# Kernel optimization log

Hardware: AMD Instinct MI355X
Metric: run time of the kernel (lower is better)

## Reference

```python
import jax, jax.numpy as jnp
import numpy as np

ND, NPR, DD, DP, LAT, AT, B = 2048, 2048, 128, 128, 128, 32, 16384


def setup_inputs():
    key = jax.random.key(0)
    ks = jax.random.split(key, 20)
    s = 0.05
    d = {}
    d["e_p_adj"] = (jax.random.uniform(ks[0], (ND, NPR)) < 0.05).astype(jnp.float32)
    d["e_e_adj"] = (jax.random.uniform(ks[1], (ND, ND)) < 0.05).astype(jnp.float32)
    d["p_p_adj"] = (jax.random.uniform(ks[2], (NPR, NPR)) < 0.05).astype(jnp.float32)
    d["input_disease"] = jax.random.randint(ks[3], (B,), 0, ND)
    d["input_drug"] = jax.random.randint(ks[4], (B,), 0, NPR)
    d["labels"] = jax.random.randint(ks[5], (B,), 0, 2)
    # learned parameters
    d["disease_emb"] = jax.random.normal(ks[6], (ND, DD)) * s
    d["drug_emb"] = jax.random.normal(ks[7], (NPR, DP)) * s
    d["Wdg"] = jax.random.normal(ks[8], (DP, LAT)) * s   # disease_gcn_w
    d["bdg_lin"] = jnp.zeros((LAT,))                      # Linear bias
    d["bdg"] = jnp.zeros((LAT,))                          # extra disease_gcn_b
    d["Wpg"] = jax.random.normal(ks[9], (DD, LAT)) * s   # drug_gcn_w
    d["bpg_lin"] = jnp.zeros((LAT,))
    d["bpg"] = jnp.zeros((LAT,))
    d["Wa1_d"] = jax.random.normal(ks[10], (DP + DD, AT)) * s  # concat [key(drug), query(disease)]
    d["ba1_d"] = jnp.zeros((AT,))
    d["Wa2_d"] = jax.random.normal(ks[11], (AT, 1)) * s
    d["ba2_d"] = jnp.zeros((1,))
    d["Wa1_p"] = jax.random.normal(ks[12], (DD + DP, AT)) * s  # concat [key(disease), query(drug)]
    d["ba1_p"] = jnp.zeros((AT,))
    d["Wa2_p"] = jax.random.normal(ks[13], (AT, 1)) * s
    d["ba2_p"] = jnp.zeros((1,))
    d["Wd2"] = jax.random.normal(ks[14], (DD, LAT)) * s  # disease_w2
    d["bd2"] = jnp.zeros((LAT,))
    d["Wp3"] = jax.random.normal(ks[15], (DP, LAT)) * s  # drug_w3
    d["bp3"] = jnp.zeros((LAT,))
    d["mlp_W1"] = jax.random.normal(ks[16], (LAT, DD)) * s
    d["mlp_b1"] = jnp.zeros((DD,))
    d["mlp_W2"] = jax.random.normal(ks[17], (DD, DD)) * s
    d["mlp_b2"] = jnp.zeros((DD,))
    d["Wpred"] = jax.random.normal(ks[18], (DD, 1)) * s
    d["bpred"] = jnp.zeros((1,))
    return d


def _attention_gcn(adj, other, selfe, W1, b1, W2, b2):
    # torch: concat([key=other, query=self]) -> Linear(W1) ; split W1 instead of
    # materializing the [Ns, No, Dk+Dq] concat tensor (same math, less HBM traffic)
    do = other.shape[1]
    ko = other @ W1[:do]              # [No, A]
    qs = selfe @ W1[do:]              # [Ns, A]
    h = jax.nn.relu(qs[:, None, :] + ko[None, :, :] + b1)   # [Ns, No, A]
    alpha = jax.nn.relu(jnp.squeeze(h @ W2, -1) + b2[0])    # [Ns, No]
    alpha = alpha * adj
    return jax.nn.softmax(alpha, axis=1) @ other            # [Ns, Do]


def _forward(e_p_adj, e_e_adj, p_p_adj, input_disease, input_drug, labels,
             disease_emb, drug_emb, Wdg, bdg_lin, bdg, Wpg, bpg_lin, bpg,
             Wa1_d, ba1_d, Wa2_d, ba2_d, Wa1_p, ba1_p, Wa2_p, ba2_p,
             Wd2, bd2, Wp3, bp3, mlp_W1, mlp_b1, mlp_W2, mlp_b2, Wpred, bpred):
    h_e_gcn = _attention_gcn(e_p_adj, drug_emb, disease_emb, Wa1_d, ba1_d, Wa2_d, ba2_d)
    h_e_gcn = h_e_gcn @ Wdg + bdg_lin + bdg
    h_p_gcn = _attention_gcn(e_p_adj.T, disease_emb, drug_emb, Wa1_p, ba1_p, Wa2_p, ba2_p)
    h_p_gcn = h_p_gcn @ Wpg + bpg_lin + bpg
    # disease knn branch
    deg_d = jnp.sum(e_e_adj, axis=1, keepdims=True) + 1e-8
    h_e_e = ((e_e_adj @ disease_emb) / deg_d) @ Wd2 + bd2
    h_e = jax.nn.selu(h_e_gcn + h_e_e)
    # drug knn branch
    deg_p = jnp.sum(p_p_adj, axis=1, keepdims=True) + 1e-8
    h_p_p = ((p_p_adj @ drug_emb) / deg_p) @ Wp3 + bp3
    h_p = jax.nn.selu(h_p_gcn + h_p_p)
    # pair prediction MLP
    x = h_e[input_disease] * h_p[input_drug]                # [B, LAT]
    x = jax.nn.selu(x @ mlp_W1 + mlp_b1)
    x = jax.nn.selu(x @ mlp_W2 + mlp_b2)
    z = jnp.squeeze(x @ Wpred, -1) + bpred[0]               # [B]
    y = labels.astype(jnp.float32)
    # BCEWithLogitsLoss (stable), mean reduction
    loss = jnp.mean(jnp.maximum(z, 0.0) - z * y + jnp.log1p(jnp.exp(-jnp.abs(z))))
    return (loss, jax.nn.sigmoid(z))


def reference(e_p_adj, e_e_adj, p_p_adj, input_disease, input_drug, labels,
              disease_emb, drug_emb, Wdg, bdg_lin, bdg, Wpg, bpg_lin, bpg,
              Wa1_d, ba1_d, Wa2_d, ba2_d, Wa1_p, ba1_p, Wa2_p, ba2_p,
              Wd2, bd2, Wp3, bp3, mlp_W1, mlp_b1, mlp_W2, mlp_b2, Wpred, bpred):
    return _forward(e_p_adj, e_e_adj, p_p_adj, input_disease, input_drug, labels,
                    disease_emb, drug_emb, Wdg, bdg_lin, bdg, Wpg, bpg_lin, bpg,
                    Wa1_d, ba1_d, Wa2_d, ba2_d, Wa1_p, ba1_p, Wa2_p, ba2_p,
                    Wd2, bd2, Wp3, bp3, mlp_W1, mlp_b1, mlp_W2, mlp_b2, Wpred, bpred)
```

## Files before the change

### kernel.cpp

```cpp
#include <hip/hip_runtime.h>

#define ND   2048
#define BB   16384

typedef unsigned short u16;
typedef unsigned int u32;
typedef __attribute__((ext_vector_type(8))) short short8;
typedef __attribute__((ext_vector_type(4))) float f32x4;

__device__ inline float bf2f(u16 u) {
    union { u32 i; float f; } v; v.i = ((u32)u) << 16; return v.f;
}
__device__ inline u16 f2bf(float f) {
    union { float f; u32 i; } v; v.f = f;
    u32 i = v.i + 0x7fffu + ((v.i >> 16) & 1u);
    return (u16)(i >> 16);
}
__device__ inline float seluf(float x) {
    const float sc = 1.0507009873554805f, al = 1.6732632423543772f;
    return x > 0.f ? sc * x : sc * al * expm1f(x);
}

__global__ void detectk(const void* __restrict__ demb, u32* __restrict__ flag,
                        u32* __restrict__ cntT, float* __restrict__ lossacc,
                        u32* __restrict__ losscnt) {
    const u16* p = (const u16*)demb;
    int tid = threadIdx.x;
    #pragma unroll
    for (int i = 0; i < 8; i++) cntT[i * 256 + tid] = 0u;
    if (tid == 0) { lossacc[0] = 0.f; losscnt[0] = 0u; }
    int sane = 0;
    #pragma unroll
    for (int i = 0; i < 2; i++) {
        u16 u = p[4 * tid + 2 * i];
        int e = (u >> 7) & 0xFF;
        if (u == 0 || (e >= 0x66 && e <= 0x8C)) sane++;
    }
    __shared__ int red[256];
    red[tid] = sane; __syncthreads();
    for (int o = 128; o > 0; o >>= 1) {
        if (tid < o) red[tid] += red[tid + o];
        __syncthreads();
    }
    if (tid == 0) flag[0] = (red[0] < 300) ? 1u : 0u;
}

#define NSEG 26
struct CvtArgs { const void* src[NSEG]; int off[NSEG]; int n[NSEG]; };
struct CS {
    const void* adj[3];
    u16* ridx[3]; u32* rcnt[3];
};

__global__ __launch_bounds__(256) void cvtcsr(CvtArgs a, u16* __restrict__ base,
                                              CS c, const u32* __restrict__ flag) {
    int bx = blockIdx.x;
    int t = threadIdx.x;
    bool f32 = flag[0] != 0;
    if (bx < 1536) {
        int m = bx >> 9;
        int r0 = (bx & 511) * 4;
        int lane = t & 63;
        __shared__ u32 lcnt[4];
        if (t < 4) lcnt[t] = 0;
        __syncthreads();
        float v[4][8];
        int c0 = t * 8;
        if (f32) {
            #pragma unroll
            for (int rr = 0; rr < 4; rr++) {
                const float4* p = (const float4*)((const float*)c.adj[m] +
                                                  (size_t)(r0 + rr) * 2048 + c0);
                float4 x = p[0], y = p[1];
                v[rr][0] = x.x; v[rr][1] = x.y; v[rr][2] = x.z; v[rr][3] = x.w;
                v[rr][4] = y.x; v[rr][5] = y.y; v[rr][6] = y.z; v[rr][7] = y.w;
            }
        } else {
            #pragma unroll
            for (int rr = 0; rr < 4; rr++) {
                const uint4* p = (const uint4*)((const u16*)c.adj[m] +
                                                (size_t)(r0 + rr) * 2048 + c0);
                uint4 x = p[0];
                u32 u[4] = {x.x, x.y, x.z, x.w};
                #pragma unroll
                for (int i = 0; i < 4; i++) {
                    v[rr][2 * i + 0] = (u[i] & 0xffffu) ? 1.f : 0.f;
                    v[rr][2 * i + 1] = (u[i] >> 16)     ? 1.f : 0.f;
                }
            }
        }
        #pragma unroll
        for (int rr = 0; rr < 4; rr++) {
            int cnt = 0;
            #pragma unroll
            for (int i = 0; i < 8; i++) cnt += (v[rr][i] != 0.f) ? 1 : 0;
            int pfx = cnt;
            #pragma unroll
            for (int o = 1; o < 64; o <<= 1) {
                int s = __shfl_up(pfx, o, 64);
                if (lane >= o) pfx += s;
            }
            int wtot = __shfl(pfx, 63, 64);
            u32 wb = 0;
            if (lane == 0) wb = atomicAdd(&lcnt[rr], (u32)wtot);
            wb = __shfl((int)wb, 0, 64);
            int o = (int)wb + pfx - cnt;
            u16* ridx = c.ridx[m] + (size_t)(r0 + rr) * 2048;
            #pragma unroll
            for (int i = 0; i < 8; i++) {
                if (v[rr][i] != 0.f) ridx[o++] = (u16)(c0 + i);
            }
        }
        __syncthreads();
        if (t < 4) c.rcnt[m][r0 + t] = lcnt[t];
    } else {
        int idx = bx - 1536;
        int seg = idx >> 6, xb = idx & 63;
        int n = a.n[seg];
        const void* s = a.src[seg];
        u16* d = base + a.off[seg];
        for (int i = xb * 256 + t; i < n; i += 16384)
            d[i] = f32 ? f2bf(((const float*)s)[i]) : ((const u16*)s)[i];
    }
}

struct PR {
    const u16* demb; const u16* pemb;
    const u16* Wa1d; const u16* ba1d;
    const u16* Wa1p; const u16* ba1p;
    float* ko_d; float* qs_d; float* ko_p; float* qs_p;
    const u16* idx0; const u32* cnt0; u16* cidx; u32* ccnt;
    const u16* ts[6]; u16* W1T; u16* W2T; u16* WcTe; u16* WcTp;
    const u16* ba[3]; const u16* bb[3]; u16* b_e; u16* b_p;
    float* csd; float* csp;
    const u16* avgidx[2]; const u32* avgcnt[2]; const u16* avgemb[2]; u16* avgout[2];
};

__global__ __launch_bounds__(256) void prep2(PR p) {
    int bx = blockIdx.x;
    int tid = threadIdx.x;
    __shared__ float sx[2][128];
    __shared__ float sred[2][128];
    __shared__ u16 stile[32][33];
    __shared__ float st0[256], st1[256];

    if (bx < 4096) {
        int sub = tid >> 7, t = tid & 127;
        int unit = bx * 2 + sub;
        int row = unit & 2047, m = unit >> 11;
        const u16* src; const u16* W; const u16* bias; float* out;
        switch (m) {
            case 0:  src = p.pemb; W = p.Wa1d;            bias = nullptr; out = p.ko_d; break;
            case 1:  src = p.demb; W = p.Wa1d + 128 * 32; bias = p.ba1d;  out = p.qs_d; break;
            case 2:  src = p.demb; W = p.Wa1p;            bias = nullptr; out = p.ko_p; break;
            default: src = p.pemb; W = p.Wa1p + 128 * 32; bias = p.ba1p;  out = p.qs_p; break;
        }
        sx[sub][t] = bf2f(src[(size_t)row * 128 + t]);
        __syncthreads();
        int a = t & 31, part = t >> 5;
        float s = 0.f;
        #pragma unroll
        for (int k = 0; k < 32; k++)
            s += sx[sub][part * 32 + k] * bf2f(W[(part * 32 + k) * 32 + a]);
        sred[sub][t] = s;
        __syncthreads();
        if (part == 0) {
            float tt = sred[sub][a] + sred[sub][a + 32] + sred[sub][a + 64] + sred[sub][a + 96];
            if (bias) tt += bf2f(bias[a]);
            out[(size_t)row * 32 + a] = tt;
        }
    } else if (bx < 6144) {
        int r = bx - 4096;
        int n = (int)p.cnt0[r];
        const u16* row = p.idx0 + (size_t)r * 2048;
        for (int i = tid; i < n; i += 256) {
            int cc = (int)row[i];
            u32 q = atomicAdd(&p.ccnt[cc], 1u);
            p.cidx[(size_t)cc * 2048 + q] = (u16)r;
        }
    } else if (bx < 6240) {
        int id = bx - 6144;
        int z = id >> 4, rem = id & 15;
        int c0 = (rem & 3) * 32, r0 = (rem >> 2) * 32;
        const u16* in = p.ts[z];
        u16* out; int ldo, ooff;
        switch (z) {
            case 0:  out = p.W1T;  ldo = 128; ooff = 0;   break;
            case 1:  out = p.W2T;  ldo = 128; ooff = 0;   break;
            case 2:  out = p.WcTe; ldo = 256; ooff = 0;   break;
            case 3:  out = p.WcTe; ldo = 256; ooff = 128; break;
            case 4:  out = p.WcTp; ldo = 256; ooff = 0;   break;
            default: out = p.WcTp; ldo = 256; ooff = 128; break;
        }
        int tx = tid & 31, ty = tid >> 5;
        int x = c0 + tx;
        for (int i = ty; i < 32; i += 8)
            stile[i][tx] = in[(size_t)(r0 + i) * 128 + x];
        __syncthreads();
        int rr = r0 + tx;
        for (int i = ty; i < 32; i += 8)
            out[(size_t)(c0 + i) * ldo + ooff + rr] = stile[tx][i];
    } else if (bx < 7264) {
        int id = bx - 6240;
        int task = id >> 9, blk = id & 511;
        int wv = tid >> 6, lane = tid & 63;
        int grp = lane >> 4, dim = lane & 15;
        int r = blk * 4 + wv;
        const u16* idx = p.avgidx[task] + (size_t)r * 2048;
        int nnz = (int)p.avgcnt[task][r];
        const u16* emb = p.avgemb[task];
        float acc[8];
        #pragma unroll
        for (int t = 0; t < 8; t++) acc[t] = 0.f;
        for (int base = 0; base < nnz; base += 64) {
            int i = base + lane;
            int j = (i < nnz) ? (int)idx[i] : 0;
            int cend = min(64, nnz - base);
            #pragma unroll 4
            for (int k4 = 0; k4 < cend; k4 += 4) {
                int kk = k4 + grp;
                int jk = __shfl(j, kk, 64);
                float wk = (base + kk < nnz) ? 1.f : 0.f;
                const uint4* pp = (const uint4*)((const char*)emb + jk * 256 + dim * 16);
                uint4 vv = *pp;
                u32 u[4] = {vv.x, vv.y, vv.z, vv.w};
                #pragma unroll
                for (int cc = 0; cc < 4; cc++) {
                    acc[2 * cc + 0] = fmaf(wk, bf2f((u16)(u[cc] & 0xffffu)), acc[2 * cc + 0]);
                    acc[2 * cc + 1] = fmaf(wk, bf2f((u16)(u[cc] >> 16)), acc[2 * cc + 1]);
                }
            }
        }
        #pragma unroll
        for (int t = 0; t < 8; t++) {
            acc[t] += __shfl_xor(acc[t], 32, 64);
            acc[t] += __shfl_xor(acc[t], 16, 64);
        }
        if (grp == 0) {
            float sc = 1.f / ((float)nnz + 1e-8f);
            float v[8];
            #pragma unroll
            for (int t = 0; t < 8; t++) v[t] = acc[t] * sc;
            uint4 pk;
            pk.x = (u32)f2bf(v[0]) | ((u32)f2bf(v[1]) << 16);
            pk.y = (u32)f2bf(v[2]) | ((u32)f2bf(v[3]) << 16);
            pk.z = (u32)f2bf(v[4]) | ((u32)f2bf(v[5]) << 16);
            pk.w = (u32)f2bf(v[6]) | ((u32)f2bf(v[7]) << 16);
            *(uint4*)(p.avgout[task] + (size_t)r * 256 + dim * 8) = pk;
        }
    } else {
        int id = bx - 7264;
        int m = id >> 1, half = id & 1;
        const u16* e = m ? p.pemb : p.demb;
        int c2 = tid & 31, rg = tid >> 5;
        int dbase = half * 64;
        float s0 = 0.f, s1 = 0.f;
        for (int it = 0; it < 256; it++) {
            int row = it * 8 + rg;
            u32 v = *(const u32*)(e + (size_t)row * 128 + dbase + c2 * 2);
            s0 += bf2f((u16)(v & 0xffffu));
            s1 += bf2f((u16)(v >> 16));
        }
        st0[tid] = s0; st1[tid] = s1;
        __syncthreads();
        if (tid < 32) {
            float a0 = 0.f, a1 = 0.f;
            #pragma unroll
            for (int g = 0; g < 8; g++) { a0 += st0[g * 32 + tid]; a1 += st1[g * 32 + tid]; }
            float* cs = m ? p.csp : p.csd;
            cs[dbase + tid * 2 + 0] = a0;
            cs[dbase + tid * 2 + 1] = a1;
        }
        if (tid < 64) {
            int d = dbase + tid;
            if (m == 0)
                p.b_e[d] = f2bf(bf2f(p.ba[0][d]) + bf2f(p.ba[1][d]) + bf2f(p.ba[2][d]));
            else
                p.b_p[d] = f2bf(bf2f(p.bb[0][d]) + bf2f(p.bb[1][d]) + bf2f(p.bb[2][d]));
        }
    }
}

struct SP {
    const u16* idx[2]; const u32* cnt[2];
    const float* ko[2]; const float* qs[2];
    const u16* w2[2]; const u16* b2[2];
    const u16* emb[2]; const float* csum[2];
    u16* out[2];
};

__global__ __launch_bounds__(256) void spagg(SP a) {
    int task = blockIdx.y;
    int tid = threadIdx.x;
    int wv = tid >> 6, lane = tid & 63;
    int grp = lane >> 4, dim = lane & 15;
    int r = blockIdx.x * 4 + wv;
    const u16* idx = a.idx[task] + (size_t)r * 2048;
    int nnz = (int)a.cnt[task][r];
    const u16* emb = a.emb[task];
    const float* ko = a.ko[task];

    float qsr[32], w2h[32];
    {
        const float4* qp = (const float4*)(a.qs[task] + (size_t)r * 32);
        #pragma unroll
        for (int i = 0; i < 8; i++) {
            float4 v = qp[i];
            qsr[4 * i + 0] = v.x; qsr[4 * i + 1] = v.y;
            qsr[4 * i + 2] = v.z; qsr[4 * i + 3] = v.w;
        }
        #pragma unroll
        for (int i = 0; i < 32; i++) w2h[i] = bf2f(a.w2[task][i]);
    }
    float b2v = bf2f(a.b2[task][0]);

    float acc[8];
    #pragma unroll
    for (int t = 0; t < 8; t++) acc[t] = 0.f;
    float wsuml = 0.f;

    for (int base = 0; base < nnz; base += 64) {
        int i = base + lane;
        float w = 0.f;
        int j = 0;
        if (i < nnz) {
            j = (int)idx[i];
            const float4* kp = (const float4*)(ko + (size_t)j * 32);
            float s = 0.f;
            #pragma unroll
            for (int q = 0; q < 8; q++) {
                float4 kv = kp[q];
                s += fmaxf(qsr[4 * q + 0] + kv.x, 0.f) * w2h[4 * q + 0];
                s += fmaxf(qsr[4 * q + 1] + kv.y, 0.f) * w2h[4 * q + 1];
                s += fmaxf(qsr[4 * q + 2] + kv.z, 0.f) * w2h[4 * q + 2];
                s += fmaxf(qsr[4 * q + 3] + kv.w, 0.f) * w2h[4 * q + 3];
            }
            w = __expf(fmaxf(s + b2v, 0.f)) - 1.f;
            wsuml += w;
        }
        int cend = min(64, nnz - base);
        #pragma unroll 4
        for (int k4 = 0; k4 < cend; k4 += 4) {
            int kk = k4 + grp;
            float wk = __shfl(w, kk, 64);
            int jk = __shfl(j, kk, 64);
            const uint4* pp = (const uint4*)((const char*)emb + jk * 256 + dim * 16);
            uint4 vv = *pp;
            u32 u[4] = {vv.x, vv.y, vv.z, vv.w};
            #pragma unroll
            for (int cc = 0; cc < 4; cc++) {
                acc[2 * cc + 0] = fmaf(wk, bf2f((u16)(u[cc] & 0xffffu)), acc[2 * cc + 0]);
                acc[2 * cc + 1] = fmaf(wk, bf2f((u16)(u[cc] >> 16)), acc[2 * cc + 1]);
            }
        }
    }

    #pragma unroll
    for (int t = 0; t < 8; t++) {
        acc[t] += __shfl_xor(acc[t], 32, 64);
        acc[t] += __shfl_xor(acc[t], 16, 64);
    }
    #pragma unroll
    for (int o = 32; o > 0; o >>= 1) wsuml += __shfl_xor(wsuml, o, 64);

    if (grp == 0) {
        float sc = 1.f / (2048.f + wsuml);
        const float* cs = a.csum[task] + dim * 8;
        float v[8];
        #pragma unroll
        for (int t = 0; t < 8; t++) v[t] = (cs[t] + acc[t]) * sc;
        uint4 pk;
        pk.x = (u32)f2bf(v[0]) | ((u32)f2bf(v[1]) << 16);
        pk.y = (u32)f2bf(v[2]) | ((u32)f2bf(v[3]) << 16);
        pk.z = (u32)f2bf(v[4]) | ((u32)f2bf(v[5]) << 16);
        pk.w = (u32)f2bf(v[6]) | ((u32)f2bf(v[7]) << 16);
        *(uint4*)(a.out[task] + (size_t)r * 256 + dim * 8) = pk;
    }
}

struct GD4 {
    const void* A[4]; const u16* BT[4]; u16* C[4];
    const u16* bias[4]; const float* rs[4];
    int lda[4], ldb[4], ldc[4], coff[4], kiters[4], act[4], araw[4], rsmode[4];
};

#define PADK 136

__global__ __launch_bounds__(256, 2) void gemmL(GD4 g, const u32* __restrict__ flag) {
    __shared__ __align__(16) u16 As[16][PADK];
    __shared__ __align__(16) u16 Bs[128][PADK];
    int z = blockIdx.y;
    const void* A = g.A[z];
    const u16* BT = g.BT[z];
    int lda = g.lda[z], ldb = g.ldb[z];
    int kiters = g.kiters[z];
    int tid = threadIdx.x;
    int lane = tid & 63, wv = tid >> 6;
    int mrow = lane & 15, quad = lane >> 4;
    int m0 = blockIdx.x * 16;
    int c0 = wv * 32;
    int sr = tid >> 4, sk = (tid & 15) * 8;
    f32x4 acc0 = {0.f, 0.f, 0.f, 0.f}, acc1 = {0.f, 0.f, 0.f, 0.f};

    short8 ra, rb[8];
    auto ldstage = [&](int kb) {
        ra = *(const short8*)((const u16*)A + (size_t)(m0 + sr) * lda + kb + sk);
        const u16* bbase = BT + (size_t)sr * ldb + kb + sk;
        #pragma unroll
        for (int i = 0; i < 8; i++)
            rb[i] = *(const short8*)(bbase + (size_t)i * 16 * ldb);
    };
    auto ststage = [&]() {
        *(short8*)(&As[sr][sk]) = ra;
        #pragma unroll
        for (int i = 0; i < 8; i++)
            *(short8*)(&Bs[i * 16 + sr][sk]) = rb[i];
    };
    auto compute = [&]() {
        #pragma unroll
        for (int ks = 0; ks < 4; ks++) {
            short8 af = *(const short8*)(&As[mrow][ks * 32 + quad * 8]);
            short8 b0 = *(const short8*)(&Bs[c0 + mrow][ks * 32 + quad * 8]);
            short8 b1 = *(const short8*)(&Bs[c0 + 16 + mrow][ks * 32 + quad * 8]);
            acc0 = __builtin_amdgcn_mfma_f32_16x16x32_bf16(af, b0, acc0, 0, 0, 0);
            acc1 = __builtin_amdgcn_mfma_f32_16x16x32_bf16(af, b1, acc1, 0, 0, 0);
        }
    };

    ldstage(0);
    #pragma unroll 1
    for (int it = 0; it < kiters - 1; ++it) {
        ststage();
        __syncthreads();
        ldstage((it + 1) * 128);
        compute();
        __syncthreads();
    }
    ststage();
    __syncthreads();
    compute();

    const float* rs = g.rs[z];
    int rsmode = g.rsmode[z];
    const u16* bi = g.bias[z];
    u16* C = g.C[z];
    int ldc = g.ldc[z], coff = g.coff[z], act = g.act[z];
    int n0 = c0 + mrow, n1 = n0 + 16;
    float bv0 = bi ? bf2f(bi[n0]) : 0.f;
    float bv1 = bi ? bf2f(bi[n1]) : 0.f;
    #pragma unroll
    for (int r = 0; r < 4; r++) {
        int row = m0 + quad * 4 + r;
        float v0 = acc0[r], v1 = acc1[r];
        if (rsmode == 1) { float sc = rs[row]; v0 *= sc; v1 *= sc; }
        else if (rsmode == 2) {
            float t = 0.f;
            #pragma unroll
            for (int p = 0; p < 8; p++) t += rs[row + p * 2048];
            float sc = 1.f / t;
            v0 *= sc; v1 *= sc;
        }
        v0 += bv0; v1 += bv1;
        if (act) { v0 = seluf(v0); v1 = seluf(v1); }
        C[(size_t)row * ldc + coff + n0] = f2bf(v0);
        C[(size_t)row * ldc + coff + n1] = f2bf(v1);
    }
}

#define PADX 136
__global__ __launch_bounds__(256, 2) void mlpfused(
    const u16* __restrict__ he, const u16* __restrict__ hp,
    const int* __restrict__ di, const int* __restrict__ dr,
    const u16* __restrict__ W1T, const u16* __restrict__ b1,
    const u16* __restrict__ W2T, const u16* __restrict__ b2,
    const u16* __restrict__ wpred, const u16* __restrict__ bpred,
    const int* __restrict__ labels,
    float* __restrict__ out, float* __restrict__ lossacc,
    u32* __restrict__ losscnt) {
    __shared__ __align__(16) u16 Xs[64][PADX];
    __shared__ __align__(16) u16 Ws[128][PADX];
    __shared__ float wred[4];
    int tid = threadIdx.x;
    int lane = tid & 63, wv = tid >> 6;
    int mrow = lane & 15, quad = lane >> 4;
    int p0 = blockIdx.x * 64;

    {
        int row = tid >> 2, sub = tid & 3;
        int b = p0 + row;
        int ia = di[b], ic = dr[b];
        const uint4* pe = (const uint4*)(he + (size_t)ia * 128 + sub * 32);
        const uint4* pp = (const uint4*)(hp + (size_t)ic * 128 + sub * 32);
        #pragma unroll
        for (int q = 0; q < 4; q++) {
            uint4 ue = pe[q], up = pp[q];
            u32 eu[4] = {ue.x, ue.y, ue.z, ue.w};
            u32 pu[4] = {up.x, up.y, up.z, up.w};
            #pragma unroll
            for (int c = 0; c < 4; c++) {
                float lo = bf2f((u16)(eu[c] & 0xffffu)) * bf2f((u16)(pu[c] & 0xffffu));
                float hi = bf2f((u16)(eu[c] >> 16)) * bf2f((u16)(pu[c] >> 16));
                *(u32*)(&Xs[row][sub * 32 + q * 8 + c * 2]) =
                    (u32)f2bf(lo) | ((u32)f2bf(hi) << 16);
            }
        }
    }
    {
        int n = tid >> 1, half = tid & 1;
        const short8* src = (const short8*)(W1T + (size_t)n * 128 + half * 64);
        short8* dst = (short8*)(&Ws[n][half * 64]);
        #pragma unroll
        for (int i = 0; i < 8; i++) dst[i] = src[i];
    }
    __syncthreads();

    f32x4 acc[8];
    #pragma unroll
    for (int nt = 0; nt < 8; nt++) acc[nt] = {0.f, 0.f, 0.f, 0.f};
    #pragma unroll
    for (int ks = 0; ks < 4; ks++) {
        short8 af = *(const short8*)(&Xs[wv * 16 + mrow][ks * 32 + quad * 8]);
        #pragma unroll
        for (int nt = 0; nt < 8; nt++) {
            short8 bfv = *(const short8*)(&Ws[nt * 16 + mrow][ks * 32 + quad * 8]);
            acc[nt] = __builtin_amdgcn_mfma_f32_16x16x32_bf16(af, bfv, acc[nt], 0, 0, 0);
        }
    }
    __syncthreads();
    #pragma unroll
    for (int nt = 0; nt < 8; nt++) {
        int col = nt * 16 + mrow;
        float bv = bf2f(b1[col]);
        #pragma unroll
        for (int r = 0; r < 4; r++) {
            int row = wv * 16 + quad * 4 + r;
            Xs[row][col] = f2bf(seluf(acc[nt][r] + bv));
        }
    }
    {
        int n = tid >> 1, half = tid & 1;
        const short8* src = (const short8*)(W2T + (size_t)n * 128 + half * 64);
        short8* dst = (short8*)(&Ws[n][half * 64]);
        #pragma unroll
        for (int i = 0; i < 8; i++) dst[i] = src[i];
    }
    __syncthreads();

    #pragma unroll
    for (int nt = 0; nt < 8; nt++) acc[nt] = {0.f, 0.f, 0.f, 0.f};
    #pragma unroll
    for (int ks = 0; ks < 4; ks++) {
        short8 af = *(const short8*)(&Xs[wv * 16 + mrow][ks * 32 + quad * 8]);
        #pragma unroll
        for (int nt = 0; nt < 8; nt++) {
            short8 bfv = *(const short8*)(&Ws[nt * 16 + mrow][ks * 32 + quad * 8]);
            acc[nt] = __builtin_amdgcn_mfma_f32_16x16x32_bf16(af, bfv, acc[nt], 0, 0, 0);
        }
    }

    float zp[4] = {0.f, 0.f, 0.f, 0.f};
    #pragma unroll
    for (int nt = 0; nt < 8; nt++) {
        int col = nt * 16 + mrow;
        float bv = bf2f(b2[col]);
        float wp = bf2f(wpred[col]);
        #pragma unroll
        for (int r = 0; r < 4; r++) {
            float x2 = bf2f(f2bf(seluf(acc[nt][r] + bv)));
            zp[r] = fmaf(x2, wp, zp[r]);
        }
    }
    #pragma unroll
    for (int r = 0; r < 4; r++) {
        #pragma unroll
        for (int o = 1; o < 16; o <<= 1) zp[r] += __shfl_xor(zp[r], o, 64);
    }
    float bpv = bf2f(bpred[0]);
    float lsum = 0.f;
    #pragma unroll
    for (int r = 0; r < 4; r++) {
        int b = p0 + wv * 16 + quad * 4 + r;
        float z = zp[r] + bpv;
        float sig = 1.f / (1.f + __expf(-z));
        if (mrow == 0) out[1 + b] = sig;
        float y = (float)labels[b];
        lsum += fmaxf(z, 0.f) - z * y + log1pf(__expf(-fabsf(z)));
    }
    lsum += __shfl_xor(lsum, 16, 64);
    lsum += __shfl_xor(lsum, 32, 64);
    if (lane == 0) wred[wv] = lsum;
    __syncthreads();
    if (tid == 0) {
        float bs = wred[0] + wred[1] + wred[2] + wred[3];
        atomicAdd(lossacc, bs);
        __threadfence();
        u32 old = atomicAdd(losscnt, 1u);
        if (old == 255u) {
            float tot = atomicAdd(lossacc, 0.f);
            out[0] = tot * (1.f / 16384.f);
        }
    }
}

extern "C" void kernel_launch(void* const* d_in, const int* in_sizes, int n_in,
                              void* d_out, int out_size, void* d_ws, size_t ws_size,
                              hipStream_t stream) {
    const void* e_p_adj = d_in[0];
    const void* e_e_adj = d_in[1];
    const void* p_p_adj = d_in[2];
    const int* in_dis  = (const int*)d_in[3];
    const int* in_drug = (const int*)d_in[4];
    const int* labels  = (const int*)d_in[5];
    float* out = (float*)d_out;

    char* ws = (char*)d_ws;
    size_t off = 0;
    auto take = [&](size_t bytes) { char* p = ws + off; off = (off + bytes + 255) & ~(size_t)255; return p; };
    u16*   A_e   = (u16*)take((size_t)2048 * 256 * 2);
    u16*   A_p   = (u16*)take((size_t)2048 * 256 * 2);
    u16*   WcTe  = (u16*)take((size_t)128 * 256 * 2);
    u16*   WcTp  = (u16*)take((size_t)128 * 256 * 2);
    u16*   W1T   = (u16*)take((size_t)128 * 128 * 2);
    u16*   W2T   = (u16*)take((size_t)128 * 128 * 2);
    u16*   b_e   = (u16*)take(256);
    u16*   b_p   = (u16*)take(256);
    u16*   h_e   = (u16*)take((size_t)2048 * 128 * 2);
    u16*   h_p   = (u16*)take((size_t)2048 * 128 * 2);
    float* ko_d  = (float*)take((size_t)2048 * 32 * 4);
    float* qs_d  = (float*)take((size_t)2048 * 32 * 4);
    float* ko_p  = (float*)take((size_t)2048 * 32 * 4);
    float* qs_p  = (float*)take((size_t)2048 * 32 * 4);
    float* csd   = (float*)take(128 * 4);
    float* csp   = (float*)take(128 * 4);
    float* lossacc = (float*)take(256);
    u32*   losscnt = (u32*)((char*)lossacc + 4);
    u32*   flag  = (u32*)take(256);
    u16*   canon = (u16*)take((size_t)700000 * 2);
    u16*   idx0  = (u16*)take((size_t)2048 * 2048 * 2);
    u16*   idx1  = (u16*)take((size_t)2048 * 2048 * 2);
    u16*   idx2  = (u16*)take((size_t)2048 * 2048 * 2);
    u16*   idx3  = (u16*)take((size_t)2048 * 2048 * 2);
    u32*   cnt0  = (u32*)take(2048 * 4);
    u32*   cnt2  = (u32*)take(2048 * 4);
    u32*   cnt3  = (u32*)take(2048 * 4);
    u32*   cntT  = (u32*)take(2048 * 4);

    const int segidx[NSEG] = {6, 7, 14, 18, 8, 22, 11, 24, 26, 28,
                              15, 16, 17, 19, 20, 21,
                              9, 10, 12, 13, 23, 25, 27, 29, 30, 31};
    const int segn[NSEG]   = {262144, 262144, 8192, 8192, 16384, 16384, 16384, 16384, 16384, 16384,
                              32, 32, 1, 32, 32, 1,
                              128, 128, 128, 128, 128, 128, 128, 128, 128, 1};
    CvtArgs ca;
    u16* cp[NSEG];
    {
        int o = 0;
        for (int i = 0; i < NSEG; i++) {
            ca.src[i] = d_in[segidx[i]];
            ca.off[i] = o;
            ca.n[i] = segn[i];
            cp[i] = canon + o;
            o += (segn[i] + 15) & ~15;
        }
    }
    u16 *cdemb = cp[0], *cpemb = cp[1], *cWa1d = cp[2], *cWa1p = cp[3];
    u16 *cWdg = cp[4], *cWd2 = cp[5], *cWpg = cp[6], *cWp3 = cp[7];
    u16 *cW1 = cp[8], *cW2 = cp[9];
    u16 *cba1d = cp[10], *cWa2d = cp[11], *cba2d = cp[12];
    u16 *cba1p = cp[13], *cWa2p = cp[14], *cba2p = cp[15];
    u16 *cbdg_lin = cp[16], *cbdg = cp[17], *cbpg_lin = cp[18], *cbpg = cp[19];
    u16 *cbd2 = cp[20], *cbp3 = cp[21], *cmb1 = cp[22], *cmb2 = cp[23];
    u16 *cWpred = cp[24], *cbpred = cp[25];

    detectk<<<1, 256, 0, stream>>>(d_in[6], flag, cntT, lossacc, losscnt);

    {
        CS cs;
        cs.adj[0] = e_p_adj; cs.ridx[0] = idx0; cs.rcnt[0] = cnt0;
        cs.adj[1] = e_e_adj; cs.ridx[1] = idx2; cs.rcnt[1] = cnt2;
        cs.adj[2] = p_p_adj; cs.ridx[2] = idx3; cs.rcnt[2] = cnt3;
        cvtcsr<<<1536 + 64 * NSEG, 256, 0, stream>>>(ca, canon, cs, flag);
    }

    PR pr;
    pr.demb = cdemb; pr.pemb = cpemb;
    pr.Wa1d = cWa1d; pr.ba1d = cba1d; pr.Wa1p = cWa1p; pr.ba1p = cba1p;
    pr.ko_d = ko_d; pr.qs_d = qs_d; pr.ko_p = ko_p; pr.qs_p = qs_p;
    pr.idx0 = idx0; pr.cnt0 = cnt0; pr.cidx = idx1; pr.ccnt = cntT;
    pr.ts[0] = cW1; pr.ts[1] = cW2; pr.ts[2] = cWdg;
    pr.ts[3] = cWd2; pr.ts[4] = cWpg; pr.ts[5] = cWp3;
    pr.W1T = W1T; pr.W2T = W2T; pr.WcTe = WcTe; pr.WcTp = WcTp;
    pr.ba[0] = cbdg_lin; pr.ba[1] = cbdg; pr.ba[2] = cbd2;
    pr.bb[0] = cbpg_lin; pr.bb[1] = cbpg; pr.bb[2] = cbp3;
    pr.b_e = b_e; pr.b_p = b_p; pr.csd = csd; pr.csp = csp;
    pr.avgidx[0] = idx2; pr.avgcnt[0] = cnt2; pr.avgemb[0] = cdemb; pr.avgout[0] = A_e + 128;
    pr.avgidx[1] = idx3; pr.avgcnt[1] = cnt3; pr.avgemb[1] = cpemb; pr.avgout[1] = A_p + 128;
    prep2<<<7268, 256, 0, stream>>>(pr);

    {
        SP sp;
        sp.idx[0] = idx0; sp.cnt[0] = cnt0; sp.ko[0] = ko_d; sp.qs[0] = qs_d;
        sp.w2[0] = cWa2d; sp.b2[0] = cba2d; sp.emb[0] = cpemb; sp.csum[0] = csp;
        sp.out[0] = A_e;
        sp.idx[1] = idx1; sp.cnt[1] = cntT; sp.ko[1] = ko_p; sp.qs[1] = qs_p;
        sp.w2[1] = cWa2p; sp.b2[1] = cba2p; sp.emb[1] = cdemb; sp.csum[1] = csd;
        sp.out[1] = A_p;
        spagg<<<dim3(512, 2), 256, 0, stream>>>(sp);
    }

    auto setd = [](GD4& g, int z, const void* A, int lda, const u16* BT, int ldb,
                   u16* C, int ldc, int coff, int ki, const u16* bi,
                   const float* rs, int act, int araw, int rm) {
        g.A[z] = A; g.lda[z] = lda; g.BT[z] = BT; g.ldb[z] = ldb;
        g.C[z] = C; g.ldc[z] = ldc; g.coff[z] = coff; g.kiters[z] = ki;
        g.bias[z] = bi; g.rs[z] = rs; g.act[z] = act; g.araw[z] = araw; g.rsmode[z] = rm;
    };

    {
        GD4 g;
        setd(g, 0, A_e, 256, WcTe, 256, h_e, 128, 0, 2, b_e, nullptr, 1, 0, 0);
        setd(g, 1, A_p, 256, WcTp, 256, h_p, 128, 0, 2, b_p, nullptr, 1, 0, 0);
        setd(g, 2, A_e, 256, WcTe, 256, h_e, 128, 0, 2, b_e, nullptr, 1, 0, 0);
        setd(g, 3, A_e, 256, WcTe, 256, h_e, 128, 0, 2, b_e, nullptr, 1, 0, 0);
        gemmL<<<dim3(128, 2), 256, 0, stream>>>(g, flag);
    }

    mlpfused<<<256, 256, 0, stream>>>(h_e, h_p, in_dis, in_drug,
                                      W1T, cmb1, W2T, cmb2,
                                      cWpred, cbpred, labels, out,
                                      lossacc, losscnt);
}
```

Measured before the change: 234.9 us.

## Fuse CSC transpose into CSR build, batch prep rows, vectorize conversion copies

Builds the transposed (column) index lists for the disease-drug adjacency directly inside the CSR conversion kernel with atomics, removing that pass from the prep kernel. The attention projection work now handles 8 rows per block with the weight matrix staged once in shared memory, instead of one block per two rows. Blocks are reordered so the long-running column-sum blocks start first, which shrinks the prep grid. The parameter conversion copy moves two elements per thread per step. Risks include more atomic contention in the conversion kernel, extra synchronisation in the batched projection loop, and a possible misaligned 32-bit access if a segment offset is odd.

After: 232.9 us. Within noise of the previous version (-0.9%).

```diff
diff --git a/kernel.cpp b/kernel.cpp
--- a/kernel.cpp
+++ b/kernel.cpp
@@ -50,6 +50,7 @@
 struct CS {
     const void* adj[3];
     u16* ridx[3]; u32* rcnt[3];
+    u16* cidx; u32* ccnt;
 };
 
 __global__ __launch_bounds__(256) void cvtcsr(CvtArgs a, u16* __restrict__ base,
@@ -108,7 +109,14 @@
             u16* ridx = c.ridx[m] + (size_t)(r0 + rr) * 2048;
             #pragma unroll
             for (int i = 0; i < 8; i++) {
-                if (v[rr][i] != 0.f) ridx[o++] = (u16)(c0 + i);
+                if (v[rr][i] != 0.f) {
+                    ridx[o++] = (u16)(c0 + i);
+                    if (m == 0) {
+                        int ccol = c0 + i;
+                        u32 q = atomicAdd(&c.ccnt[ccol], 1u);
+                        c.cidx[(size_t)ccol * 2048 + q] = (u16)(r0 + rr);
+                    }
+                }
             }
         }
         __syncthreads();
@@ -119,8 +127,21 @@
         int n = a.n[seg];
         const void* s = a.src[seg];
         u16* d = base + a.off[seg];
-        for (int i = xb * 256 + t; i < n; i += 16384)
-            d[i] = f32 ? f2bf(((const float*)s)[i]) : ((const u16*)s)[i];
+        int nw = n >> 1;
+        if (f32) {
+            const float2* sf = (const float2*)s;
+            u32* dw = (u32*)d;
+            for (int i = xb * 256 + t; i < nw; i += 16384) {
+                float2 v = sf[i];
+                dw[i] = (u32)f2bf(v.x) | ((u32)f2bf(v.y) << 16);
+            }
+        } else {
+            const u32* sw = (const u32*)s;
+            u32* dw = (u32*)d;
+            for (int i = xb * 256 + t; i < nw; i += 16384) dw[i] = sw[i];
+        }
+        if ((n & 1) && xb == 0 && t == 0)
+            d[n - 1] = f32 ? f2bf(((const float*)s)[n - 1]) : ((const u16*)s)[n - 1];
     }
 }
 
@@ -129,7 +150,6 @@
     const u16* Wa1d; const u16* ba1d;
     const u16* Wa1p; const u16* ba1p;
     float* ko_d; float* qs_d; float* ko_p; float* qs_p;
-    const u16* idx0; const u32* cnt0; u16* cidx; u32* ccnt;
     const u16* ts[6]; u16* W1T; u16* W2T; u16* WcTe; u16* WcTp;
     const u16* ba[3]; const u16* bb[3]; u16* b_e; u16* b_p;
     float* csd; float* csp;
@@ -143,65 +163,40 @@
     __shared__ float sred[2][128];
     __shared__ u16 stile[32][33];
     __shared__ float st0[256], st1[256];
-
-    if (bx < 4096) {
-        int sub = tid >> 7, t = tid & 127;
-        int unit = bx * 2 + sub;
-        int row = unit & 2047, m = unit >> 11;
-        const u16* src; const u16* W; const u16* bias; float* out;
-        switch (m) {
-            case 0:  src = p.pemb; W = p.Wa1d;            bias = nullptr; out = p.ko_d; break;
-            case 1:  src = p.demb; W = p.Wa1d + 128 * 32; bias = p.ba1d;  out = p.qs_d; break;
-            case 2:  src = p.demb; W = p.Wa1p;            bias = nullptr; out = p.ko_p; break;
-            default: src = p.pemb; W = p.Wa1p + 128 * 32; bias = p.ba1p;  out = p.qs_p; break;
-        }
-        sx[sub][t] = bf2f(src[(size_t)row * 128 + t]);
+    __shared__ u16 Wl[4096];
+
+    if (bx < 4) {
+        int id = bx;
+        int m = id >> 1, half = id & 1;
+        const u16* e = m ? p.pemb : p.demb;
+        int c2 = tid & 31, rg = tid >> 5;
+        int dbase = half * 64;
+        float s0 = 0.f, s1 = 0.f;
+        for (int it = 0; it < 256; it++) {
+            int row = it * 8 + rg;
+            u32 v = *(const u32*)(e + (size_t)row * 128 + dbase + c2 * 2);
+            s0 += bf2f((u16)(v & 0xffffu));
+            s1 += bf2f((u16)(v >> 16));
+        }
+        st0[tid] = s0; st1[tid] = s1;
         __syncthreads();
-        int a = t & 31, part = t >> 5;
-        float s = 0.f;
-        #pragma unroll
-        for (int k = 0; k < 32; k++)
-            s += sx[sub][part * 32 + k] * bf2f(W[(part * 32 + k) * 32 + a]);
-        sred[sub][t] = s;
-        __syncthreads();
-        if (part == 0) {
-            float tt = sred[sub][a] + sred[sub][a + 32] + sred[sub][a + 64] + sred[sub][a + 96];
-            if (bias) tt += bf2f(bias[a]);
-            out[(size_t)row * 32 + a] = tt;
-        }
-    } else if (bx < 6144) {
-        int r = bx - 4096;
-        int n = (int)p.cnt0[r];
-        const u16* row = p.idx0 + (size_t)r * 2048;
-        for (int i = tid; i < n; i += 256) {
-            int cc = (int)row[i];
-            u32 q = atomicAdd(&p.ccnt[cc], 1u);
-            p.cidx[(size_t)cc * 2048 + q] = (u16)r;
-        }
-    } else if (bx < 6240) {
-        int id = bx - 6144;
-        int z = id >> 4, rem = id & 15;
-        int c0 = (rem & 3) * 32, r0 = (rem >> 2) * 32;
-        const u16* in = p.ts[z];
-        u16* out; int ldo, ooff;
-        switch (z) {
-            case 0:  out = p.W1T;  ldo = 128; ooff = 0;   break;
-            case 1:  out = p.W2T;  ldo = 128; ooff = 0;   break;
-            case 2:  out = p.WcTe; ldo = 256; ooff = 0;   break;
-            case 3:  out = p.WcTe; ldo = 256; ooff = 128; break;
-            case 4:  out = p.WcTp; ldo = 256; ooff = 0;   break;
-            default: out = p.WcTp; ldo = 256; ooff = 128; break;
-        }
-        int tx = tid & 31, ty = tid >> 5;
-        int x = c0 + tx;
-        for (int i = ty; i < 32; i += 8)
-            stile[i][tx] = in[(size_t)(r0 + i) * 128 + x];
-        __syncthreads();
-        int rr = r0 + tx;
-        for (int i = ty; i < 32; i += 8)
-            out[(size_t)(c0 + i) * ldo + ooff + rr] = stile[tx][i];
-    } else if (bx < 7264) {
-        int id = bx - 6240;
+        if (tid < 32) {
+            float a0 = 0.f, a1 = 0.f;
+            #pragma unroll
+            for (int g = 0; g < 8; g++) { a0 += st0[g * 32 + tid]; a1 += st1[g * 32 + tid]; }
+            float* cs = m ? p.csp : p.csd;
+            cs[dbase + tid * 2 + 0] = a0;
+            cs[dbase + tid * 2 + 1] = a1;
+        }
+        if (tid < 64) {
+            int d = dbase + tid;
+            if (m == 0)
+                p.b_e[d] = f2bf(bf2f(p.ba[0][d]) + bf2f(p.ba[1][d]) + bf2f(p.ba[2][d]));
+            else
+                p.b_p[d] = f2bf(bf2f(p.bb[0][d]) + bf2f(p.bb[1][d]) + bf2f(p.bb[2][d]));
+        }
+    } else if (bx < 1028) {
+        int id = bx - 4;
         int task = id >> 9, blk = id & 511;
         int wv = tid >> 6, lane = tid & 63;
         int grp = lane >> 4, dim = lane & 15;
@@ -248,36 +243,66 @@
             pk.w = (u32)f2bf(v[6]) | ((u32)f2bf(v[7]) << 16);
             *(uint4*)(p.avgout[task] + (size_t)r * 256 + dim * 8) = pk;
         }
+    } else if (bx < 2052) {
+        int blk = bx - 1028;
+        int m = blk >> 8;
+        int r0 = (blk & 255) * 8;
+        const u16* src; const u16* W; const u16* bias; float* out;
+        switch (m) {
+            case 0:  src = p.pemb; W = p.Wa1d;            bias = nullptr; out = p.ko_d; break;
+            case 1:  src = p.demb; W = p.Wa1d + 128 * 32; bias = p.ba1d;  out = p.qs_d; break;
+            case 2:  src = p.demb; W = p.Wa1p;            bias = nullptr; out = p.ko_p; break;
+            default: src = p.pemb; W = p.Wa1p + 128 * 32; bias = p.ba1p;  out = p.qs_p; break;
+        }
+        {
+            const uint4* wsrc = (const uint4*)W;
+            uint4* wdst = (uint4*)Wl;
+            #pragma unroll
+            for (int i = 0; i < 2; i++) wdst[i * 256 + tid] = wsrc[i * 256 + tid];
+        }
+        __syncthreads();
+        int sub = tid >> 7, t = tid & 127;
+        int a = t & 31, part = t >> 5;
+        #pragma unroll 1
+        for (int rp = 0; rp < 4; rp++) {
+            int row = r0 + rp * 2 + sub;
+            sx[sub][t] = bf2f(src[(size_t)row * 128 + t]);
+            __syncthreads();
+            float s = 0.f;
+            #pragma unroll
+            for (int k = 0; k < 32; k++)
+                s += sx[sub][part * 32 + k] * bf2f(Wl[(part * 32 + k) * 32 + a]);
+            sred[sub][t] = s;
+            __syncthreads();
+            if (part == 0) {
+                float tt = sred[sub][a] + sred[sub][a + 32] + sred[sub][a + 64] + sred[sub][a + 96];
+                if (bias) tt += bf2f(bias[a]);
+                out[(size_t)row * 32 + a] = tt;
+            }
+            __syncthreads();
+        }
     } else {
-        int id = bx - 7264;
-        int m = id >> 1, half = id & 1;
-        const u16* e = m ? p.pemb : p.demb;
-        int c2 = tid & 31, rg = tid >> 5;
-        int dbase = half * 64;
-        float s0 = 0.f, s1 = 0.f;
-        for (int it = 0; it < 256; it++) {
-            int row = it * 8 + rg;
-            u32 v = *(const u32*)(e + (size_t)row * 128 + dbase + c2 * 2);
-            s0 += bf2f((u16)(v & 0xffffu));
-            s1 += bf2f((u16)(v >> 16));
-        }
-        st0[tid] = s0; st1[tid] = s1;
+        int id = bx - 2052;
+        int z = id >> 4, rem = id & 15;
+        int c0 = (rem & 3) * 32, r0 = (rem >> 2) * 32;
+        const u16* in = p.ts[z];
+        u16* out; int ldo, ooff;
+        switch (z) {
+            case 0:  out = p.W1T;  ldo = 128; ooff = 0;   break;
+            case 1:  out = p.W2T;  ldo = 128; ooff = 0;   break;
+            case 2:  out = p.WcTe; ldo = 256; ooff = 0;   break;
+            case 3:  out = p.WcTe; ldo = 256; ooff = 128; break;
+            case 4:  out = p.WcTp; ldo = 256; ooff = 0;   break;
+            default: out = p.WcTp; ldo = 256; ooff = 128; break;
+        }
+        int tx = tid & 31, ty = tid >> 5;
+        int x = c0 + tx;
+        for (int i = ty; i < 32; i += 8)
+            stile[i][tx] = in[(size_t)(r0 + i) * 128 + x];
         __syncthreads();
-        if (tid < 32) {
-            float a0 = 0.f, a1 = 0.f;
-            #pragma unroll
-            for (int g = 0; g < 8; g++) { a0 += st0[g * 32 + tid]; a1 += st1[g * 32 + tid]; }
-            float* cs = m ? p.csp : p.csd;
-            cs[dbase + tid * 2 + 0] = a0;
-            cs[dbase + tid * 2 + 1] = a1;
-        }
-        if (tid < 64) {
-            int d = dbase + tid;
-            if (m == 0)
-                p.b_e[d] = f2bf(bf2f(p.ba[0][d]) + bf2f(p.ba[1][d]) + bf2f(p.ba[2][d]));
-            else
-                p.b_p[d] = f2bf(bf2f(p.bb[0][d]) + bf2f(p.bb[1][d]) + bf2f(p.bb[2][d]));
-        }
+        int rr = r0 + tx;
+        for (int i = ty; i < 32; i += 8)
+            out[(size_t)(c0 + i) * ldo + ooff + rr] = stile[tx][i];
     }
 }
 
@@ -679,6 +704,7 @@
         cs.adj[0] = e_p_adj; cs.ridx[0] = idx0; cs.rcnt[0] = cnt0;
         cs.adj[1] = e_e_adj; cs.ridx[1] = idx2; cs.rcnt[1] = cnt2;
         cs.adj[2] = p_p_adj; cs.ridx[2] = idx3; cs.rcnt[2] = cnt3;
+        cs.cidx = idx1; cs.ccnt = cntT;
         cvtcsr<<<1536 + 64 * NSEG, 256, 0, stream>>>(ca, canon, cs, flag);
     }
 
@@ -686,7 +712,6 @@
     pr.demb = cdemb; pr.pemb = cpemb;
     pr.Wa1d = cWa1d; pr.ba1d = cba1d; pr.Wa1p = cWa1p; pr.ba1p = cba1p;
     pr.ko_d = ko_d; pr.qs_d = qs_d; pr.ko_p = ko_p; pr.qs_p = qs_p;
-    pr.idx0 = idx0; pr.cnt0 = cnt0; pr.cidx = idx1; pr.ccnt = cntT;
     pr.ts[0] = cW1; pr.ts[1] = cW2; pr.ts[2] = cWdg;
     pr.ts[3] = cWd2; pr.ts[4] = cWpg; pr.ts[5] = cWp3;
     pr.W1T = W1T; pr.W2T = W2T; pr.WcTe = WcTe; pr.WcTp = WcTp;
@@ -695,7 +720,7 @@
     pr.b_e = b_e; pr.b_p = b_p; pr.csd = csd; pr.csp = csp;
     pr.avgidx[0] = idx2; pr.avgcnt[0] = cnt2; pr.avgemb[0] = cdemb; pr.avgout[0] = A_e + 128;
     pr.avgidx[1] = idx3; pr.avgcnt[1] = cnt3; pr.avgemb[1] = cpemb; pr.avgout[1] = A_p + 128;
-    prep2<<<7268, 256, 0, stream>>>(pr);
+    prep2<<<2148, 256, 0, stream>>>(pr);
 
     {
         SP sp;
```
